# Optimization experiments

Hardware: AMD Instinct MI355X
Metric: run time of the kernel (lower is better)

Reference implementation:

```python
import jax, jax.numpy as jnp
import numpy as np


def _lsa(cost):
    """Exact rectangular linear sum assignment (Jonker-Volgenant / e-maxx
    Hungarian with potentials). Returns (row_ind, col_ind) matching
    scipy.optimize.linear_sum_assignment (row_ind sorted ascending)."""
    n, m = cost.shape
    transposed = n > m
    if transposed:
        cost = cost.T
        n, m = m, n
    cost = np.asarray(cost, dtype=np.float64)
    INF = 1e18
    u = np.zeros(n + 1)
    v = np.zeros(m + 1)
    p = np.zeros(m + 1, dtype=np.int64)   # p[j]: 1-based row assigned to col j
    way = np.zeros(m + 1, dtype=np.int64)
    for i in range(1, n + 1):
        p[0] = i
        j0 = 0
        minv = np.full(m + 1, INF)
        used = np.zeros(m + 1, dtype=bool)
        while True:
            used[j0] = True
            i0 = p[j0]
            cur = cost[i0 - 1] - u[i0] - v[1:]          # vectorized over cols
            upd = (~used[1:]) & (cur < minv[1:])
            minv[1:] = np.where(upd, cur, minv[1:])
            way[1:] = np.where(upd, j0, way[1:])
            masked = np.where(used[1:], INF, minv[1:])
            j1 = int(np.argmin(masked)) + 1
            delta = masked[j1 - 1]
            u[p[used]] += delta
            v[used] -= delta
            minv[1:] = np.where(used[1:], minv[1:], minv[1:] - delta)
            j0 = j1
            if p[j0] == 0:
                break
        while j0 != 0:
            j1 = way[j0]
            p[j0] = p[j1]
            j0 = j1
    if transposed:
        pairs = sorted((j - 1, p[j] - 1) for j in range(1, m + 1) if p[j] != 0)
    else:
        pairs = sorted((p[j] - 1, j - 1) for j in range(1, m + 1) if p[j] != 0)
    row_ind = np.array([r for r, _ in pairs], dtype=np.int64)
    col_ind = np.array([c for _, c in pairs], dtype=np.int64)
    return row_ind, col_ind


def _row_order(cost_b):
    """Matched rows first (scipy order), then unmatched rows sorted ascending."""
    N = cost_b.shape[0]
    row_ind, _ = _lsa(cost_b)
    remain = sorted(set(range(N)) - set(row_ind.tolist()))
    return np.concatenate([row_ind, np.asarray(remain, dtype=np.int64)])


def _pairwise_l2(seq1, seq2):
    # Fused batched cdist: ||a-b|| = sqrt(|a|^2 + |b|^2 - 2 a.b)
    a2 = jnp.sum(seq1 * seq1, axis=-1)[:, :, None]   # [B,N,1]
    b2 = jnp.sum(seq2 * seq2, axis=-1)[:, None, :]   # [B,1,M]
    ab = jnp.einsum('bnd,bmd->bnm', seq1, seq2)      # [B,N,M]
    return jnp.sqrt(jnp.maximum(a2 + b2 - 2.0 * ab, 0.0))


def setup_inputs() -> dict:
    key = jax.random.key(0)
    k1, k2 = jax.random.split(key)
    B, N, M, D = 16, 512, 448, 1536
    return {
        'seq1': jax.random.normal(k1, (B, N, D), dtype=jnp.float32),
        'seq2': jax.random.normal(k2, (B, M, D), dtype=jnp.float32),
    }


def reference(seq1, seq2):
    cost = np.asarray(_pairwise_l2(seq1, seq2))      # [B,N,M], one fused kernel
    # Hungarian solve is inherently sequential / CPU-bound per batch element.
    perm = np.stack([_row_order(cost[b]) for b in range(cost.shape[0])], 0)
    perm = jnp.asarray(perm)                         # [B,N]
    return jnp.take_along_axis(seq1, perm[:, :, None], axis=1)
```

## Files before the change

### kernel.cpp

```cpp
#include <hip/hip_runtime.h>
#include <math.h>

#define BB 16
#define NN 512
#define MM 448
#define DD 1536

constexpr int TK = 32;

__global__ __launch_bounds__(256) void cost_kernel(const float* __restrict__ s1,
                                                   const float* __restrict__ s2,
                                                   float* __restrict__ Ct) {
  __shared__ float As[TK][68];
  __shared__ float Bs[TK][68];
  const int b = blockIdx.z;
  const int ibase = blockIdx.x * 64;
  const int jbase = blockIdx.y * 64;
  const int tid = threadIdx.x;
  const float* s1b = s1 + ((size_t)b * NN + ibase) * DD;
  const float* s2b = s2 + ((size_t)b * MM + jbase) * DD;
  const int ix = (tid & 15) * 4;
  const int jy = (tid >> 4) * 4;
  double acc[16];
#pragma unroll
  for (int t = 0; t < 16; ++t) acc[t] = 0.0;

  for (int k0 = 0; k0 < DD; k0 += TK) {
#pragma unroll
    for (int rep = 0; rep < 2; ++rep) {
      int idx = tid + rep * 256;
      int r = idx >> 3;
      int c4 = (idx & 7) * 4;
      float4 a = *(const float4*)(s1b + (size_t)r * DD + k0 + c4);
      As[c4 + 0][r] = a.x; As[c4 + 1][r] = a.y; As[c4 + 2][r] = a.z; As[c4 + 3][r] = a.w;
      float4 bb = *(const float4*)(s2b + (size_t)r * DD + k0 + c4);
      Bs[c4 + 0][r] = bb.x; Bs[c4 + 1][r] = bb.y; Bs[c4 + 2][r] = bb.z; Bs[c4 + 3][r] = bb.w;
    }
    __syncthreads();
    float pacc[16];
#pragma unroll
    for (int t = 0; t < 16; ++t) pacc[t] = 0.f;
#pragma unroll 8
    for (int kk = 0; kk < TK; ++kk) {
      float4 av = *(const float4*)&As[kk][ix];
      float4 bv = *(const float4*)&Bs[kk][jy];
      float a[4] = {av.x, av.y, av.z, av.w};
      float bq[4] = {bv.x, bv.y, bv.z, bv.w};
#pragma unroll
      for (int t = 0; t < 4; ++t)
#pragma unroll
        for (int q = 0; q < 4; ++q) {
          float d = a[t] - bq[q];
          pacc[t * 4 + q] = fmaf(d, d, pacc[t * 4 + q]);
        }
    }
#pragma unroll
    for (int t = 0; t < 16; ++t) acc[t] += (double)pacc[t];
    __syncthreads();
  }
#pragma unroll
  for (int t = 0; t < 4; ++t)
#pragma unroll
    for (int q = 0; q < 4; ++q) {
      int i = ibase + ix + t;
      int jj = jbase + jy + q;
      float d2 = (float)acc[t * 4 + q];
      Ct[((size_t)b * MM + jj) * NN + i] = sqrtf(fmaxf(d2, 0.f));
    }
}

__device__ __forceinline__ unsigned wave_min_bcast_u32(unsigned x) {
  int v = (int)x;
#define ST(C) { int o = __builtin_amdgcn_update_dpp(-1, v, C, 0xF, 0xF, false); \
                v = ((unsigned)o < (unsigned)v) ? o : v; }
  ST(0x111) ST(0x112) ST(0x114) ST(0x118) ST(0x142) ST(0x143)
#undef ST
  return (unsigned)__builtin_amdgcn_readlane(v, 63);
}

__device__ __forceinline__ float wave_min_bcast_f32(float x) {
  union FU { float f; int i; };
  FU v; v.f = x;
  const int INFB = 0x7f7fffff;
#define DPP1(CTRL) { FU o; \
  o.i = __builtin_amdgcn_update_dpp(INFB, v.i, CTRL, 0xF, 0xF, false); \
  if (o.f < v.f) v.f = o.f; }
  DPP1(0x111) DPP1(0x112) DPP1(0x114) DPP1(0x118) DPP1(0x142) DPP1(0x143)
#undef DPP1
  FU r; r.i = __builtin_amdgcn_readlane(v.i, 63);
  return r.f;
}

__device__ __forceinline__ double readlane_f64(double x, int sl) {
  union { double d; int i[2]; } v, r;
  v.d = x;
  r.i[0] = __builtin_amdgcn_readlane(v.i[0], sl);
  r.i[1] = __builtin_amdgcn_readlane(v.i[1], sl);
  return r.d;
}

__device__ __forceinline__ void exact_min_sl(double x, double& mn, int& sl) {
  float xf = (float)x;
  float rf = wave_min_bcast_f32(xf);
  unsigned long long bm = __ballot(xf == rf);
  if (__popcll(bm) == 1) {
    sl = (int)__ffsll(bm) - 1;
    mn = readlane_f64(x, sl);
  } else {
    union { double d; unsigned u[2]; } v, r;
    v.d = x;
    unsigned hmin = wave_min_bcast_u32(v.u[1]);
    unsigned lc = (v.u[1] == hmin) ? v.u[0] : 0xFFFFFFFFu;
    unsigned lmin = wave_min_bcast_u32(lc);
    unsigned long long b2 = __ballot((v.u[1] == hmin) && (v.u[0] == lmin));
    sl = (int)__ffsll(b2) - 1;
    r.u[0] = lmin; r.u[1] = hmin;
    mn = r.d;
  }
}

__global__ __launch_bounds__(64) void jv_kernel(const float* __restrict__ Ct,
                                                int* __restrict__ perm) {
  const int b = blockIdx.x;
  const float* C = Ct + (size_t)b * MM * NN;
  __shared__ double u_lds[MM + 1];
  __shared__ int p_lds[NN + 1];
  __shared__ int way_lds[NN + 1];
  __shared__ double rec_lds[NN + 1];
  __shared__ int preg_lds[NN + 1];
  __shared__ int colOwner[NN];
  __shared__ int rowMatched[MM];
  __shared__ int freeL[MM];
  __shared__ int nfree_s;
  __shared__ int cnt_lds[64];
  const int lane = threadIdx.x;
  const int jbase = 8 * lane + 1;

  if (lane == 0) u_lds[0] = 0.0;
  for (int t = lane; t <= NN; t += 64) { p_lds[t] = 0; way_lds[t] = 0; }
  for (int t = lane; t < NN; t += 64) colOwner[t] = -1;
  for (int t = lane; t < MM; t += 64) rowMatched[t] = 0;
  asm volatile("s_waitcnt lgkmcnt(0)" ::: "memory");

  {
    const float4* r40 = (const float4*)(C);
    const float4* r41 = (const float4*)(C + (size_t)NN);
    float4 ca = r40[2 * lane], cb = r40[2 * lane + 1];
    float4 na = r41[2 * lane], nb = r41[2 * lane + 1];
    for (int r = 0; r < MM; ++r) {
      int rp = (r + 2 < MM) ? (r + 2) : (MM - 1);
      const float4* r4n = (const float4*)(C + (size_t)rp * NN);
      float4 pa = r4n[2 * lane], pb = r4n[2 * lane + 1];
      float c[8] = {ca.x, ca.y, ca.z, ca.w, cb.x, cb.y, cb.z, cb.w};
      float lm = 1e30f; int la = 0;
#pragma unroll
      for (int q = 0; q < 8; ++q)
        if (c[q] < lm) { lm = c[q]; la = 8 * lane + q; }
      float rm = wave_min_bcast_f32(lm);
      unsigned long long bm = __ballot(lm == rm);
      int sl = (int)__ffsll((unsigned long long)bm) - 1;
      int jc = __builtin_amdgcn_readlane(la, sl);
      if (lane == 0) {
        u_lds[r + 1] = (double)rm;
        if (colOwner[jc] < 0) {
          colOwner[jc] = r;
          rowMatched[r] = 1;
          p_lds[jc + 1] = r + 1;
        }
      }
      ca = na; cb = nb; na = pa; nb = pb;
    }
  }
  double vcol[8];
#pragma unroll
  for (int q = 0; q < 8; ++q) vcol[q] = 0.0;
  asm volatile("s_waitcnt lgkmcnt(0)" ::: "memory");

  if (lane == 0) {
    int n = 0;
    for (int r = 0; r < MM; ++r) if (!rowMatched[r]) freeL[n++] = r;
    nfree_s = n;
  }
  asm volatile("s_waitcnt lgkmcnt(0)" ::: "memory");
  int nfree = nfree_s;

  for (int pass = 0; pass < 4; ++pass) {
    int prev = nfree; nfree = 0; int k = 0;
    if (prev == 0) continue;
    int i = freeL[0];
    {
      const float4* r4p = (const float4*)(C + (size_t)i * NN);
      float4 ca = r4p[2 * lane];
      float4 cb = r4p[2 * lane + 1];
      while (true) {
        const int kn = k + 1;
        const int ig = (kn < prev) ? freeL[kn] : 0;
        const float4* r4n = (const float4*)(C + (size_t)ig * NN);
        float4 nca = r4n[2 * lane];
        float4 ncb = r4n[2 * lane + 1];

        float c[8] = {ca.x, ca.y, ca.z, ca.w, cb.x, cb.y, cb.z, cb.w};
        double m1 = 1e18, m2 = 1e18; int a1 = 0;
#pragma unroll
        for (int q = 0; q < 8; ++q) {
          double h = (double)c[q] - vcol[q];
          if (h < m1) { m2 = m1; m1 = h; a1 = 8 * lane + q; }
          else if (h < m2) m2 = h;
        }
        double umin; int sl;
        exact_min_sl(m1, umin, sl);
        int j1 = __builtin_amdgcn_readlane(a1, sl);
        double cd = (lane == sl) ? m2 : m1;
        double usub; int sl2;
        exact_min_sl(cd, usub, sl2);
        const bool strict = (umin < usub);
        if (strict && (j1 >> 3) == lane) {
          double dec = usub - umin;
#pragma unroll
          for (int qq = 0; qq < 8; ++qq) if (qq == (j1 & 7)) vcol[qq] -= dec;
        }
        const int powner = p_lds[j1 + 1];
        asm volatile("" ::: "memory");
        const int i0 = powner - 1;
        if (lane == 0) { u_lds[i + 1] = usub; p_lds[j1 + 1] = i + 1; }
        const bool reproc = (i0 >= 0) && strict;
        if (i0 >= 0 && !strict) {
          if (lane == 0) freeL[nfree] = i0;
          nfree++;
        }
        asm volatile("s_waitcnt lgkmcnt(0)" ::: "memory");
        if (reproc) {
          i = i0;
          const float4* r4m = (const float4*)(C + (size_t)i * NN);
          ca = r4m[2 * lane];
          cb = r4m[2 * lane + 1];
        } else {
          k = kn;
          if (k >= prev) break;
          i = ig; ca = nca; cb = ncb;
        }
      }
    }
  }

  const int nf3 = nfree;
  for (int fi = 0; fi < nf3; ++fi) {
    const int i = freeL[fi] + 1;
    if (lane == 0) p_lds[0] = i;
    double minv[8], coff[8];
    int wayr[8];
#pragma unroll
    for (int q = 0; q < 8; ++q) { minv[q] = 1e18; coff[q] = 0.0; wayr[q] = 0; }
    double cum = 0.0;
    int j0 = 0;
    asm volatile("s_waitcnt lgkmcnt(0)" ::: "memory");

    const float4* r4p = (const float4*)(C + (size_t)(i - 1) * NN);
    float4 na = r4p[2 * lane];
    float4 nb = r4p[2 * lane + 1];
    double uu = u_lds[i];

    while (true) {
      float c8[8] = {na.x, na.y, na.z, na.w, nb.x, nb.y, nb.z, nb.w};
#pragma unroll
      for (int q = 0; q < 8; ++q) {
        double cur = (((double)c8[q] - uu) - vcol[q]) + coff[q];
        cur = (cur > 0.0) ? cur : 0.0;
        bool imp = cur < minv[q];
        minv[q] = imp ? cur : minv[q];
        wayr[q] = imp ? j0 : wayr[q];
      }
      double m01 = (minv[1] < minv[0]) ? minv[1] : minv[0];
      int    a01 = (minv[1] < minv[0]) ? jbase + 1 : jbase + 0;
      double m23 = (minv[3] < minv[2]) ? minv[3] : minv[2];
      int    a23 = (minv[3] < minv[2]) ? jbase + 3 : jbase + 2;
      double m45 = (minv[5] < minv[4]) ? minv[5] : minv[4];
      int    a45 = (minv[5] < minv[4]) ? jbase + 5 : jbase + 4;
      double m67 = (minv[7] < minv[6]) ? minv[7] : minv[6];
      int    a67 = (minv[7] < minv[6]) ? jbase + 7 : jbase + 6;
      double m03 = (m23 < m01) ? m23 : m01;
      int    a03 = (m23 < m01) ? a23 : a01;
      double m47 = (m67 < m45) ? m67 : m45;
      int    a47 = (m67 < m45) ? a67 : a45;
      double lm = (m47 < m03) ? m47 : m03;
      int    la = (m47 < m03) ? a47 : a03;

      int pcand = p_lds[la];

      float lmf = (float)lm;
      float rmf = wave_min_bcast_f32(lmf);
      unsigned long long bmf = __ballot(lmf == rmf);
      int slp = (int)__ffsll(bmf) - 1;
      int j1 = __builtin_amdgcn_readlane(la, slp);
      int pn = __builtin_amdgcn_readlane(pcand, slp);
      int rs = (pn > 0) ? (pn - 1) : 0;
      const float4* r4s = (const float4*)(C + (size_t)rs * NN);
      float4 sca = r4s[2 * lane];
      float4 scb = r4s[2 * lane + 1];
      double uus = u_lds[pn];

      double delta;
      if (__popcll(bmf) == 1) {
        delta = readlane_f64(lm, slp);
      } else {
        union { double d; unsigned u[2]; } lv, dd;
        lv.d = lm;
        unsigned hmin = wave_min_bcast_u32(lv.u[1]);
        unsigned lc = (lv.u[1] == hmin) ? lv.u[0] : 0xFFFFFFFFu;
        unsigned lmin = wave_min_bcast_u32(lc);
        unsigned long long bm2 = __ballot((lv.u[1] == hmin) && (lv.u[0] == lmin));
        int sl = (int)__ffsll(bm2) - 1;
        dd.u[0] = lmin; dd.u[1] = hmin;
        delta = dd.d;
        if (sl != slp) {
          j1 = __builtin_amdgcn_readlane(la, sl);
          pn = __builtin_amdgcn_readlane(pcand, sl);
          int rs2 = (pn > 0) ? (pn - 1) : 0;
          const float4* r4m = (const float4*)(C + (size_t)rs2 * NN);
          sca = r4m[2 * lane];
          scb = r4m[2 * lane + 1];
          uus = u_lds[pn];
        }
      }
      cum += delta;
#pragma unroll
      for (int q = 0; q < 8; ++q) minv[q] -= delta;
      j0 = j1;
      if (pn == 0) break;

      na = sca; nb = scb; uu = uus;

      {
        const int ow = (j1 - 1) >> 3;
        const int qs = (j1 - 1) & 7;
#pragma unroll
        for (int q = 0; q < 8; ++q) if (qs == q) {
          bool me = (lane == ow);
          minv[q] = me ? 5e17 : minv[q];
          coff[q] = me ? 1e18 : coff[q];
        }
        if (lane == 0) { rec_lds[j1] = cum; preg_lds[j1] = pn; }
      }
    }

    if (lane == 0) u_lds[i] += cum;
    asm volatile("s_waitcnt lgkmcnt(0)" ::: "memory");
#pragma unroll
    for (int q = 0; q < 8; ++q) {
      way_lds[jbase + q] = wayr[q];
      if (coff[q] != 0.0) {
        double d = cum - rec_lds[jbase + q];
        int pr = preg_lds[jbase + q];
        vcol[q] -= d;
        u_lds[pr] += d;
      }
    }
    asm volatile("s_waitcnt lgkmcnt(0)" ::: "memory");
    if (lane == 0) {
      int jj = j0;
      while (jj != 0) { int jp = way_lds[jj]; p_lds[jj] = p_lds[jp]; jj = jp; }
    }
    asm volatile("s_waitcnt lgkmcnt(0)" ::: "memory");
  }

  int mask = 0, cnt = 0;
#pragma unroll
  for (int q = 0; q < 8; ++q)
    if (p_lds[jbase + q] != 0) { mask |= 1 << q; cnt++; }
  cnt_lds[lane] = cnt;
  asm volatile("s_waitcnt lgkmcnt(0)" ::: "memory");
  int pre = 0;
  for (int l = 0; l < 64; ++l) { int cl = cnt_lds[l]; if (l < lane) pre += cl; }
  int mpos = pre;
  int upos = MM + (8 * lane - pre);
#pragma unroll
  for (int q = 0; q < 8; ++q) {
    int col = 8 * lane + q;
    if ((mask >> q) & 1) perm[b * NN + mpos++] = col;
    else                 perm[b * NN + upos++] = col;
  }
}

__global__ __launch_bounds__(256) void gather_kernel(const float* __restrict__ s1,
                                                     const int* __restrict__ perm,
                                                     float* __restrict__ out) {
  const int bi = blockIdx.x;
  const int b = bi >> 9;
  const int src = perm[bi];
  const float4* sp = (const float4*)(s1 + ((size_t)b * NN + src) * DD);
  float4* dp = (float4*)(out + (size_t)bi * DD);
  for (int t = threadIdx.x; t < DD / 4; t += 256) dp[t] = sp[t];
}

extern "C" void kernel_launch(void* const* d_in, const int* in_sizes, int n_in,
                              void* d_out, int out_size, void* d_ws, size_t ws_size,
                              hipStream_t stream) {
  const float* s1 = (const float*)d_in[0];
  const float* s2 = (const float*)d_in[1];
  float* out = (float*)d_out;
  float* Ct = (float*)d_out;
  int* perm = (int*)d_ws;

  dim3 cg(NN / 64, MM / 64, BB);
  cost_kernel<<<cg, 256, 0, stream>>>(s1, s2, Ct);
  jv_kernel<<<BB, 64, 0, stream>>>(Ct, perm);
  gather_kernel<<<BB * NN, 256, 0, stream>>>(s1, perm, out);
}
```

Baseline: 6.977 ms.

## Use unconditional exact f64 wave-min and halve auction passes in JV solver

Replaces the float-first, ballot-branching exact-min helper with an unconditional two-stage u32 DPP min over the double's high and low words. The solver still speculatively prefetches the row picked by the float min, and reloads only if the exact argmin names a different owner. The min trees use fmin, and the initial auction/reduction passes drop from 4 to 2, which shortens preprocessing but leaves more free rows for the augmenting phase. The intent is to remove divergent branches and shorten the serial critical path of each Dijkstra step. The cost is always paying for two DPP reductions plus a ballot.

```diff
diff --git a/kernel.cpp b/kernel.cpp
--- a/kernel.cpp
+++ b/kernel.cpp
@@ -78,6 +78,16 @@
   return (unsigned)__builtin_amdgcn_readlane(v, 63);
 }
 
+__device__ __forceinline__ double wave_min_bcast_f64_fast(double x) {
+  union DU { double d; unsigned u[2]; };
+  DU v; v.d = x;
+  unsigned hmin = wave_min_bcast_u32(v.u[1]);
+  unsigned lc = (v.u[1] == hmin) ? v.u[0] : 0xFFFFFFFFu;
+  unsigned lmin = wave_min_bcast_u32(lc);
+  DU r; r.u[0] = lmin; r.u[1] = hmin;
+  return r.d;
+}
+
 __device__ __forceinline__ float wave_min_bcast_f32(float x) {
   union FU { float f; int i; };
   FU v; v.f = x;
@@ -89,34 +99,6 @@
 #undef DPP1
   FU r; r.i = __builtin_amdgcn_readlane(v.i, 63);
   return r.f;
-}
-
-__device__ __forceinline__ double readlane_f64(double x, int sl) {
-  union { double d; int i[2]; } v, r;
-  v.d = x;
-  r.i[0] = __builtin_amdgcn_readlane(v.i[0], sl);
-  r.i[1] = __builtin_amdgcn_readlane(v.i[1], sl);
-  return r.d;
-}
-
-__device__ __forceinline__ void exact_min_sl(double x, double& mn, int& sl) {
-  float xf = (float)x;
-  float rf = wave_min_bcast_f32(xf);
-  unsigned long long bm = __ballot(xf == rf);
-  if (__popcll(bm) == 1) {
-    sl = (int)__ffsll(bm) - 1;
-    mn = readlane_f64(x, sl);
-  } else {
-    union { double d; unsigned u[2]; } v, r;
-    v.d = x;
-    unsigned hmin = wave_min_bcast_u32(v.u[1]);
-    unsigned lc = (v.u[1] == hmin) ? v.u[0] : 0xFFFFFFFFu;
-    unsigned lmin = wave_min_bcast_u32(lc);
-    unsigned long long b2 = __ballot((v.u[1] == hmin) && (v.u[0] == lmin));
-    sl = (int)__ffsll(b2) - 1;
-    r.u[0] = lmin; r.u[1] = hmin;
-    mn = r.d;
-  }
 }
 
 __global__ __launch_bounds__(64) void jv_kernel(const float* __restrict__ Ct,
@@ -184,7 +166,7 @@
   asm volatile("s_waitcnt lgkmcnt(0)" ::: "memory");
   int nfree = nfree_s;
 
-  for (int pass = 0; pass < 4; ++pass) {
+  for (int pass = 0; pass < 2; ++pass) {
     int prev = nfree; nfree = 0; int k = 0;
     if (prev == 0) continue;
     int i = freeL[0];
@@ -207,12 +189,12 @@
           if (h < m1) { m2 = m1; m1 = h; a1 = 8 * lane + q; }
           else if (h < m2) m2 = h;
         }
-        double umin; int sl;
-        exact_min_sl(m1, umin, sl);
+        double umin = wave_min_bcast_f64_fast(m1);
+        unsigned long long bm = __ballot(m1 == umin);
+        int sl = (int)__ffsll((unsigned long long)bm) - 1;
         int j1 = __builtin_amdgcn_readlane(a1, sl);
         double cd = (lane == sl) ? m2 : m1;
-        double usub; int sl2;
-        exact_min_sl(cd, usub, sl2);
+        double usub = wave_min_bcast_f64_fast(cd);
         const bool strict = (umin < usub);
         if (strict && (j1 >> 3) == lane) {
           double dec = usub - umin;
@@ -267,22 +249,22 @@
         double cur = (((double)c8[q] - uu) - vcol[q]) + coff[q];
         cur = (cur > 0.0) ? cur : 0.0;
         bool imp = cur < minv[q];
-        minv[q] = imp ? cur : minv[q];
         wayr[q] = imp ? j0 : wayr[q];
-      }
-      double m01 = (minv[1] < minv[0]) ? minv[1] : minv[0];
+        minv[q] = fmin(cur, minv[q]);
+      }
+      double m01 = fmin(minv[0], minv[1]);
       int    a01 = (minv[1] < minv[0]) ? jbase + 1 : jbase + 0;
-      double m23 = (minv[3] < minv[2]) ? minv[3] : minv[2];
+      double m23 = fmin(minv[2], minv[3]);
       int    a23 = (minv[3] < minv[2]) ? jbase + 3 : jbase + 2;
-      double m45 = (minv[5] < minv[4]) ? minv[5] : minv[4];
+      double m45 = fmin(minv[4], minv[5]);
       int    a45 = (minv[5] < minv[4]) ? jbase + 5 : jbase + 4;
-      double m67 = (minv[7] < minv[6]) ? minv[7] : minv[6];
+      double m67 = fmin(minv[6], minv[7]);
       int    a67 = (minv[7] < minv[6]) ? jbase + 7 : jbase + 6;
-      double m03 = (m23 < m01) ? m23 : m01;
+      double m03 = fmin(m01, m23);
       int    a03 = (m23 < m01) ? a23 : a01;
-      double m47 = (m67 < m45) ? m67 : m45;
+      double m47 = fmin(m45, m67);
       int    a47 = (m67 < m45) ? a67 : a45;
-      double lm = (m47 < m03) ? m47 : m03;
+      double lm = fmin(m03, m47);
       int    la = (m47 < m03) ? a47 : a03;
 
       int pcand = p_lds[la];
@@ -291,44 +273,38 @@
       float rmf = wave_min_bcast_f32(lmf);
       unsigned long long bmf = __ballot(lmf == rmf);
       int slp = (int)__ffsll(bmf) - 1;
-      int j1 = __builtin_amdgcn_readlane(la, slp);
-      int pn = __builtin_amdgcn_readlane(pcand, slp);
-      int rs = (pn > 0) ? (pn - 1) : 0;
+      int pnf = __builtin_amdgcn_readlane(pcand, slp);
+      int rs = (pnf > 0) ? (pnf - 1) : 0;
       const float4* r4s = (const float4*)(C + (size_t)rs * NN);
       float4 sca = r4s[2 * lane];
       float4 scb = r4s[2 * lane + 1];
-      double uus = u_lds[pn];
-
-      double delta;
-      if (__popcll(bmf) == 1) {
-        delta = readlane_f64(lm, slp);
-      } else {
-        union { double d; unsigned u[2]; } lv, dd;
-        lv.d = lm;
-        unsigned hmin = wave_min_bcast_u32(lv.u[1]);
-        unsigned lc = (lv.u[1] == hmin) ? lv.u[0] : 0xFFFFFFFFu;
-        unsigned lmin = wave_min_bcast_u32(lc);
-        unsigned long long bm2 = __ballot((lv.u[1] == hmin) && (lv.u[0] == lmin));
-        int sl = (int)__ffsll(bm2) - 1;
-        dd.u[0] = lmin; dd.u[1] = hmin;
-        delta = dd.d;
-        if (sl != slp) {
-          j1 = __builtin_amdgcn_readlane(la, sl);
-          pn = __builtin_amdgcn_readlane(pcand, sl);
-          int rs2 = (pn > 0) ? (pn - 1) : 0;
-          const float4* r4m = (const float4*)(C + (size_t)rs2 * NN);
-          sca = r4m[2 * lane];
-          scb = r4m[2 * lane + 1];
-          uus = u_lds[pn];
-        }
-      }
+      double uus = u_lds[pnf];
+
+      union DU { double d; unsigned u[2]; } lv, dd;
+      lv.d = lm;
+      unsigned hmin = wave_min_bcast_u32(lv.u[1]);
+      unsigned lc = (lv.u[1] == hmin) ? lv.u[0] : 0xFFFFFFFFu;
+      unsigned lmin = wave_min_bcast_u32(lc);
+      unsigned long long bm2 = __ballot((lv.u[1] == hmin) && (lv.u[0] == lmin));
+      int sl = (int)__ffsll(bm2) - 1;
+      int j1 = __builtin_amdgcn_readlane(la, sl);
+      int pn = __builtin_amdgcn_readlane(pcand, sl);
+      dd.u[0] = lmin; dd.u[1] = hmin;
+      double delta = dd.d;
       cum += delta;
 #pragma unroll
       for (int q = 0; q < 8; ++q) minv[q] -= delta;
       j0 = j1;
       if (pn == 0) break;
 
-      na = sca; nb = scb; uu = uus;
+      if (pn == pnf) {
+        na = sca; nb = scb; uu = uus;
+      } else {
+        const float4* r4m = (const float4*)(C + (size_t)(pn - 1) * NN);
+        na = r4m[2 * lane];
+        nb = r4m[2 * lane + 1];
+        uu = u_lds[pn];
+      }
 
       {
         const int ow = (j1 - 1) >> 3;
```

New measurement: 6.424 ms. 1.09x faster.
